# Kernel tuning notes

Measured on AMD Instinct MI355X. Metric: run time of the kernel, lower is better.

The kernel has to match this reference:

```python
import jax, jax.numpy as jnp
import numpy as np

N_NODES = 100000
N_EDGES = 1600000
F_IN, F_HID, F_OUT = 128, 128, 16
NEG_SLOPE = 0.2


def _glorot(key, shape):
    fan = sum(shape)
    return jax.random.uniform(key, shape, jnp.float32, -1.0, 1.0) * jnp.sqrt(6.0 / fan)


def setup_inputs() -> dict:
    key = jax.random.key(0)
    ks = jax.random.split(key, 16)
    x = jax.random.normal(ks[0], (N_NODES, F_IN), jnp.float32)
    edge_index = jax.random.randint(ks[1], (2, N_EDGES), 0, N_NODES, jnp.int64)
    d1, d2, d3 = F_HID, F_HID // 2, F_OUT
    return {
        'x': x,
        'edge_index': edge_index,
        'W1': _glorot(ks[2], (F_IN, d1)), 'a_src1': _glorot(ks[3], (d1,)), 'a_dst1': _glorot(ks[4], (d1,)), 'b1': jnp.zeros((d1,), jnp.float32),
        'W2': _glorot(ks[5], (d1, d2)), 'a_src2': _glorot(ks[6], (d2,)), 'a_dst2': _glorot(ks[7], (d2,)), 'b2': jnp.zeros((d2,), jnp.float32),
        'W3': _glorot(ks[8], (d2, d3)), 'a_src3': _glorot(ks[9], (d3,)), 'a_dst3': _glorot(ks[10], (d3,)), 'b3': jnp.zeros((d3,), jnp.float32),
    }


def gat_conv(x, src, dst, W, a_s, a_d, b):
    # x: [N, Fin] -> h: [N, Fout]; src/dst: [E] (self-loops included)
    h = x @ W
    e = jax.nn.leaky_relu(h @ a_s, NEG_SLOPE * 0 + NEG_SLOPE)  # placeholder avoided below
    # attention logits per edge: leaky_relu(alpha_src[src] + alpha_dst[dst])
    al_s = h @ a_s  # [N]
    al_d = h @ a_d  # [N]
    logits = jax.nn.leaky_relu(al_s[src] + al_d[dst], NEG_SLOPE)  # [E]
    # numerically stable softmax over incoming edges of each dst node
    m = jax.ops.segment_max(logits, dst, num_segments=N_NODES)
    m = jnp.where(jnp.isfinite(m), m, 0.0)
    ex = jnp.exp(logits - m[dst])
    denom = jax.ops.segment_sum(ex, dst, num_segments=N_NODES)
    alpha = ex / denom[dst]  # self-loops guarantee denom > 0
    out = jax.ops.segment_sum(alpha[:, None] * h[src], dst, num_segments=N_NODES)
    return out + b


def reference(x, edge_index, W1, a_src1, a_dst1, b1, W2, a_src2, a_dst2, b2, W3, a_src3, a_dst3, b3):
    loops = jnp.arange(N_NODES, dtype=edge_index.dtype)
    src = jnp.concatenate([edge_index[0], loops])
    dst = jnp.concatenate([edge_index[1], loops])
    h = gat_conv(x, src, dst, W1, a_src1, a_dst1, b1)
    h = jax.nn.relu(h)  # dropout p=0.5 is identity in eval mode
    h = gat_conv(h, src, dst, W2, a_src2, a_dst2, b2)
    h = jax.nn.relu(h)
    out = gat_conv(h, src, dst, W3, a_src3, a_dst3, b3)
    return out
```

## Files before the change

kernel.cpp:

```cpp
#include <hip/hip_runtime.h>
#include <hip/hip_bf16.h>

typedef __hip_bfloat16 bf16;
typedef __attribute__((ext_vector_type(8))) __bf16 bf16x8;
typedef __attribute__((ext_vector_type(4))) float f32x4;

static constexpr int N = 100000;
static constexpr int E = 1600000;
static constexpr int ETOT = E + N;
static constexpr float SLOPE = 0.2f;

__device__ __constant__ int c_poff[12] = {0, 16384, 16512, 16640,
                                          16768, 24960, 25024, 25088,
                                          25152, 26176, 26192, 26208};
static constexpr int PTOT = 26224;
static constexpr int H_POFF[12] = {0, 16384, 16512, 16640, 16768, 24960,
                                   25024, 25088, 25152, 26176, 26192, 26208};

struct Src12 { const void* p[12]; };

__device__ __forceinline__ float bfLo(unsigned u) { return __uint_as_float(u << 16); }
__device__ __forceinline__ float bfHi(unsigned u) { return __uint_as_float(u & 0xFFFF0000u); }

__device__ __forceinline__ void fma8(const uint4 r, float e, float* acc) {
  acc[0] = fmaf(e, bfLo(r.x), acc[0]);
  acc[1] = fmaf(e, bfHi(r.x), acc[1]);
  acc[2] = fmaf(e, bfLo(r.y), acc[2]);
  acc[3] = fmaf(e, bfHi(r.y), acc[3]);
  acc[4] = fmaf(e, bfLo(r.z), acc[4]);
  acc[5] = fmaf(e, bfHi(r.z), acc[5]);
  acc[6] = fmaf(e, bfLo(r.w), acc[6]);
  acc[7] = fmaf(e, bfHi(r.w), acc[7]);
}

__device__ __forceinline__ float edge_ex(float l) {
  l = (l > 0.f) ? l : SLOPE * l;
  return __expf(l);
}

__device__ __forceinline__ void loadEdge(const int* __restrict__ ei32,
                                         const long long* __restrict__ ei64,
                                         int use64, int t, int& s, int& d) {
  if (t >= E) { s = d = t - E; return; }
  if (use64) { s = (int)ei64[t]; d = (int)ei64[E + t]; }
  else       { s = ei32[t];      d = ei32[E + t]; }
}

__device__ __forceinline__ unsigned pk2(float a, float b) {
  bf16 x = __float2bfloat16(a), y = __float2bfloat16(b);
  unsigned short ux = *(unsigned short*)&x, uy = *(unsigned short*)&y;
  return ((unsigned)uy << 16) | ux;
}

static constexpr int CHUNK = 8192;
static constexpr int NCHK  = (ETOT + CHUNK - 1) / CHUNK;
static constexpr int NB1   = (N + 511) / 512;
static constexpr int M1    = NB1 * NCHK;
static constexpr int SBLK  = (M1 + 255) / 256;

__global__ __launch_bounds__(256) void detect_kernel(
    const unsigned long long* __restrict__ ei64,
    const unsigned short* __restrict__ w1u16, int* __restrict__ flags) {
  const int t = threadIdx.x;
  __shared__ unsigned long long bl[4];
  __shared__ unsigned long long sb64;
  const int w = t >> 6;
  bool p64 = (t < 64) && (ei64[t] >= (unsigned long long)N);
  unsigned long long b64 = __ballot(p64);
  if (t == 0) sb64 = b64;
  bool pf = (((w1u16[t] >> 7) & 0xFFu) >= 126u);
  unsigned long long bf_ = __ballot(pf);
  if ((t & 63) == 0) bl[w] = bf_;
  __syncthreads();
  if (t == 0) {
    flags[0] = (sb64 == 0ull) ? 1 : 0;
    flags[1] = ((bl[0] | bl[1] | bl[2] | bl[3]) != 0ull) ? 1 : 0;
  }
}

static constexpr int PB_PAR = (PTOT + 255) / 256;
static constexpr int PB_W1  = 128 * 128 / 256;
static constexpr int PB_W2  = 128 * 64 / 256;
static constexpr int PB_W3  = 64 * 16 / 256;
static constexpr int PB_TOT = NCHK + PB_PAR + PB_W1 + PB_W2 + PB_W3;

__device__ __forceinline__ void conv_w(const void* W, int kd, int dout, int f32,
                                       bf16* __restrict__ wt, int idx) {
  int n = idx / kd, k = idx - n * kd;
  float v = f32 ? ((const float*)W)[k * dout + n]
                : __bfloat162float(((const bf16*)W)[k * dout + n]);
  wt[idx] = __float2bfloat16(v);
}

__global__ __launch_bounds__(256) void prep_kernel(
    const int* __restrict__ ei32, const long long* __restrict__ ei64,
    const int* __restrict__ flags, int* __restrict__ c1,
    Src12 s, float* __restrict__ prm,
    bf16* __restrict__ w1t, bf16* __restrict__ w2t, bf16* __restrict__ w3t) {
  const int b = blockIdx.x, tid = threadIdx.x;
  const int f64 = flags[0], f32 = flags[1];
  if (b < NCHK) {
    __shared__ int h1[NB1];
    if (tid < NB1) h1[tid] = 0;
    __syncthreads();
    const int t0 = b * CHUNK;
#pragma unroll 4
    for (int i = tid; i < CHUNK; i += 256) {
      int t = t0 + i;
      if (t < ETOT) {
        int d = (t >= E) ? (t - E) : (f64 ? (int)ei64[E + t] : ei32[E + t]);
        atomicAdd(&h1[d >> 9], 1);
      }
    }
    __syncthreads();
    if (tid < NB1) c1[tid * NCHK + b] = h1[tid];
  } else if (b < NCHK + PB_PAR) {
    int t = (b - NCHK) * 256 + tid;
    if (t < PTOT) {
      int k = 0;
#pragma unroll
      for (int i = 1; i < 12; ++i)
        if (t >= c_poff[i]) k = i;
      int j = t - c_poff[k];
      prm[t] = f32 ? ((const float*)s.p[k])[j]
                   : __bfloat162float(((const bf16*)s.p[k])[j]);
    }
  } else if (b < NCHK + PB_PAR + PB_W1) {
    conv_w(s.p[0], 128, 128, f32, w1t, (b - NCHK - PB_PAR) * 256 + tid);
  } else if (b < NCHK + PB_PAR + PB_W1 + PB_W2) {
    conv_w(s.p[4], 128, 64, f32, w2t, (b - NCHK - PB_PAR - PB_W1) * 256 + tid);
  } else {
    conv_w(s.p[8], 64, 16, f32, w3t, (b - NCHK - PB_PAR - PB_W1 - PB_W2) * 256 + tid);
  }
}

__global__ __launch_bounds__(256) void scanA_kernel(const int* __restrict__ c1,
                                                    int* __restrict__ bsum) {
  __shared__ int red[256];
  const int t = threadIdx.x;
  const int i = blockIdx.x * 256 + t;
  red[t] = (i < M1) ? c1[i] : 0;
  __syncthreads();
#pragma unroll
  for (int off = 128; off > 0; off >>= 1) {
    if (t < off) red[t] += red[t + off];
    __syncthreads();
  }
  if (t == 0) bsum[blockIdx.x] = red[0];
}

__global__ __launch_bounds__(256) void scanB_kernel(const int* __restrict__ bsum,
                                                    int* __restrict__ boff) {
  __shared__ int s[256];
  const int t = threadIdx.x;
  const int v = (t < SBLK) ? bsum[t] : 0;
  s[t] = v;
  __syncthreads();
  for (int off = 1; off < 256; off <<= 1) {
    int u = (t >= off) ? s[t - off] : 0;
    __syncthreads();
    s[t] += u;
    __syncthreads();
  }
  if (t < SBLK) boff[t] = s[t] - v;
}

__global__ __launch_bounds__(256) void scanC_kernel(const int* __restrict__ c1,
                                                    const int* __restrict__ boff,
                                                    int* __restrict__ off1) {
  __shared__ int s[256];
  const int t = threadIdx.x;
  const int i = blockIdx.x * 256 + t;
  const int v = (i < M1) ? c1[i] : 0;
  s[t] = v;
  __syncthreads();
#pragma unroll
  for (int off = 1; off < 256; off <<= 1) {
    int u = (t >= off) ? s[t - off] : 0;
    __syncthreads();
    s[t] += u;
    __syncthreads();
  }
  if (i < M1) off1[i] = boff[blockIdx.x] + s[t] - v;
}

__device__ __forceinline__ void phaseC_body(int c, const int* __restrict__ ei32,
                                            const long long* __restrict__ ei64,
                                            int f64, const int* __restrict__ off1,
                                            int2* __restrict__ tmp) {
  __shared__ int cur[NB1];
  const int tid = threadIdx.x;
  if (tid < NB1) cur[tid] = off1[tid * NCHK + c];
  __syncthreads();
  const int t0 = c * CHUNK;
#pragma unroll 4
  for (int i = tid; i < CHUNK; i += 256) {
    int t = t0 + i;
    if (t < ETOT) {
      int s, d;
      loadEdge(ei32, ei64, f64, t, s, d);
      int pos = atomicAdd(&cur[d >> 9], 1);
      tmp[pos] = make_int2(d, s);
    }
  }
}

__global__ __launch_bounds__(256) void phaseD_kernel(const int* __restrict__ off1,
                                                     const int2* __restrict__ tmp,
                                                     int* __restrict__ rowptr,
                                                     int* __restrict__ ssrt,
                                                     const float* __restrict__ als1,
                                                     const float* __restrict__ ald1,
                                                     float* __restrict__ exf) {
  __shared__ int h2[512], e2[512], cur[512];
  __shared__ int ps[256];
  const int b = blockIdx.x, t = threadIdx.x;
  const int base = off1[b * NCHK];
  const int end = (b + 1 < NB1) ? off1[(b + 1) * NCHK] : ETOT;
  const int len = end - base;
  h2[2 * t] = 0; h2[2 * t + 1] = 0;
  __syncthreads();
  for (int i = t; i < len; i += 256)
    atomicAdd(&h2[tmp[base + i].x & 511], 1);
  __syncthreads();
  const int s1 = h2[2 * t], s2 = h2[2 * t + 1];
  ps[t] = s1 + s2;
  __syncthreads();
  for (int off = 1; off < 256; off <<= 1) {
    int u = (t >= off) ? ps[t - off] : 0;
    __syncthreads();
    ps[t] += u;
    __syncthreads();
  }
  const int ep = ps[t] - (s1 + s2);
  e2[2 * t] = ep;
  e2[2 * t + 1] = ep + s1;
  cur[2 * t] = ep;
  cur[2 * t + 1] = ep + s1;
  __syncthreads();
#pragma unroll
  for (int k = 0; k < 2; ++k) {
    int f = 2 * t + k;
    int node = (b << 9) + f;
    if (node < N) rowptr[node] = base + e2[f];
  }
  if (b == 0 && t == 0) rowptr[N] = ETOT;
  for (int i = t; i < len; i += 256) {
    int2 e = tmp[base + i];
    int pos = base + atomicAdd(&cur[e.x & 511], 1);
    ssrt[pos] = e.y;
    exf[pos] = edge_ex(als1[e.y] + ald1[e.x]);
  }
}

template <int KD, int DOUT, bool XD>
__device__ __forceinline__ void gemm_body(int bb, const void* __restrict__ inv,
                                          const int* __restrict__ flags,
                                          const unsigned short* __restrict__ wt,
                                          bf16* __restrict__ h,
                                          const float* __restrict__ a_s,
                                          const float* __restrict__ a_d,
                                          float* __restrict__ als,
                                          float* __restrict__ ald) {
  constexpr int SA = KD + 8;
  constexpr int NT = DOUT / 16;
  constexpr int KS = KD / 32;
  __shared__ unsigned short sA[64 * SA];
  __shared__ unsigned short sB[DOUT * SA];
  const int tid = threadIdx.x;
  const int m0 = bb * 64;
  for (int idx = tid; idx < DOUT * KD / 8; idx += 256) {
    int n = idx / (KD / 8), k8 = idx - n * (KD / 8);
    *(uint4*)(sB + n * SA + k8 * 8) = *(const uint4*)(wt + n * KD + k8 * 8);
  }
  const bool f32 = XD ? (flags[1] != 0) : false;
  for (int idx = tid; idx < 64 * KD / 8; idx += 256) {
    int r = idx / (KD / 8), k8 = idx - r * (KD / 8);
    int m = m0 + r;
    uint4 v = make_uint4(0, 0, 0, 0);
    if (m < N) {
      if (XD && f32) {
        const float4 v0 = *((const float4*)inv + ((size_t)m * KD + k8 * 8) / 4);
        const float4 v1 = *((const float4*)inv + ((size_t)m * KD + k8 * 8) / 4 + 1);
        v = make_uint4(pk2(v0.x, v0.y), pk2(v0.z, v0.w),
                       pk2(v1.x, v1.y), pk2(v1.z, v1.w));
      } else {
        v = *((const uint4*)inv + ((size_t)m * KD + k8 * 8) / 8);
      }
    }
    *(uint4*)(sA + r * SA + k8 * 8) = v;
  }
  __syncthreads();
  const int lane = tid & 63;
  const int wv = tid >> 6;
  const int lr = lane & 15;
  const int q = lane >> 4;
  f32x4 acc[NT];
#pragma unroll
  for (int t = 0; t < NT; ++t)
#pragma unroll
    for (int r = 0; r < 4; ++r) acc[t][r] = 0.f;
  const int arow = wv * 16 + lr;
#pragma unroll
  for (int ks = 0; ks < KS; ++ks) {
    const int k0 = ks * 32 + q * 8;
    const bf16x8 a = *(const bf16x8*)(sA + arow * SA + k0);
#pragma unroll
    for (int t = 0; t < NT; ++t) {
      const bf16x8 b = *(const bf16x8*)(sB + (t * 16 + lr) * SA + k0);
      acc[t] = __builtin_amdgcn_mfma_f32_16x16x32_bf16(a, b, acc[t], 0, 0, 0);
    }
  }
  float ps[4] = {0.f, 0.f, 0.f, 0.f}, pd[4] = {0.f, 0.f, 0.f, 0.f};
#pragma unroll
  for (int t = 0; t < NT; ++t) {
    const float av = a_s[t * 16 + lr];
    const float dv = a_d[t * 16 + lr];
#pragma unroll
    for (int r = 0; r < 4; ++r) {
      ps[r] = fmaf(acc[t][r], av, ps[r]);
      pd[r] = fmaf(acc[t][r], dv, pd[r]);
    }
  }
#pragma unroll
  for (int m = 1; m < 16; m <<= 1)
#pragma unroll
    for (int r = 0; r < 4; ++r) {
      ps[r] += __shfl_xor(ps[r], m, 64);
      pd[r] += __shfl_xor(pd[r], m, 64);
    }
  const int mb = m0 + wv * 16 + q * 4;
  if (lr == 0) {
#pragma unroll
    for (int r = 0; r < 4; ++r) {
      int m = mb + r;
      if (m < N) { als[m] = ps[r]; ald[m] = pd[r]; }
    }
  }
#pragma unroll
  for (int t = 0; t < NT; ++t)
#pragma unroll
    for (int r = 0; r < 4; ++r) {
      int m = mb + r;
      if (m < N) h[(size_t)m * DOUT + t * 16 + lr] = __float2bfloat16(acc[t][r]);
    }
}

static constexpr int GB1 = (N + 63) / 64;

__global__ __launch_bounds__(256) void gemm1_phaseC(
    const void* __restrict__ x, const int* __restrict__ flags,
    const unsigned short* __restrict__ wt, bf16* __restrict__ h,
    const float* __restrict__ a_s, const float* __restrict__ a_d,
    float* __restrict__ als, float* __restrict__ ald,
    const int* __restrict__ ei32, const long long* __restrict__ ei64,
    const int* __restrict__ off1, int2* __restrict__ tmp) {
  if (blockIdx.x < GB1) {
    gemm_body<128, 128, true>(blockIdx.x, x, flags, wt, h, a_s, a_d, als, ald);
  } else {
    int c = blockIdx.x - GB1;
    if (c < NCHK) phaseC_body(c, ei32, ei64, flags[0], off1, tmp);
  }
}

static constexpr int AB = (N + 127) / 128;

template <int DA, int DOUT, bool EXF>
__global__ __launch_bounds__(512) void aggemm_kernel(
    const int* __restrict__ rowptr, const int* __restrict__ ssrt,
    const float* __restrict__ exf,
    const float* __restrict__ als_in, const float* __restrict__ ald_in,
    const unsigned short* __restrict__ hin, const float* __restrict__ bias,
    const unsigned short* __restrict__ wt, bf16* __restrict__ hout,
    const float* __restrict__ a_s, const float* __restrict__ a_d,
    float* __restrict__ als_out, float* __restrict__ ald_out) {
  constexpr int SA = DA + 8;
  constexpr int TPN = DA / 8;
  constexpr int NPR = 512 / TPN;
  constexpr int NR = 128 / NPR;
  constexpr int NT = DOUT / 16;
  constexpr int KS = DA / 32;
  __shared__ unsigned short sA[128 * SA];
  const int tid = threadIdx.x;
  const int m0 = blockIdx.x * 128;
  const int sub = tid % TPN;
  const int rr0 = tid / TPN;
  const int col0 = sub * 8;
#pragma unroll
  for (int r = 0; r < NR; ++r) {
    const int row = r * NPR + rr0;
    const int d = m0 + row;
    if (d < N) {
      const int p0 = rowptr[d], p1 = rowptr[d + 1];
      const float ad = EXF ? 0.f : ald_in[d];
      float acc[8];
#pragma unroll
      for (int c = 0; c < 8; ++c) acc[c] = 0.f;
      float sum = 0.f;
      int p = p0;
      for (; p + 4 <= p1; p += 4) {
        const int s0 = ssrt[p + 0];
        const int s1 = ssrt[p + 1];
        const int s2 = ssrt[p + 2];
        const int s3 = ssrt[p + 3];
        const uint4 r0 = *reinterpret_cast<const uint4*>(hin + (size_t)s0 * DA + col0);
        const uint4 r1 = *reinterpret_cast<const uint4*>(hin + (size_t)s1 * DA + col0);
        const uint4 r2 = *reinterpret_cast<const uint4*>(hin + (size_t)s2 * DA + col0);
        const uint4 r3 = *reinterpret_cast<const uint4*>(hin + (size_t)s3 * DA + col0);
        const float x0 = EXF ? exf[p + 0] : edge_ex(als_in[s0] + ad);
        const float x1 = EXF ? exf[p + 1] : edge_ex(als_in[s1] + ad);
        const float x2 = EXF ? exf[p + 2] : edge_ex(als_in[s2] + ad);
        const float x3 = EXF ? exf[p + 3] : edge_ex(als_in[s3] + ad);
        sum += (x0 + x1) + (x2 + x3);
        fma8(r0, x0, acc);
        fma8(r1, x1, acc);
        fma8(r2, x2, acc);
        fma8(r3, x3, acc);
      }
      for (; p < p1; ++p) {
        const int s = ssrt[p];
        const uint4 rr = *reinterpret_cast<const uint4*>(hin + (size_t)s * DA + col0);
        const float x = EXF ? exf[p] : edge_ex(als_in[s] + ad);
        sum += x;
        fma8(rr, x, acc);
      }
      const float inv = 1.f / sum;
      float v[8];
#pragma unroll
      for (int c = 0; c < 8; ++c) {
        float w = acc[c] * inv + bias[col0 + c];
        v[c] = (w > 0.f) ? w : 0.f;
      }
      uint4 pk = make_uint4(pk2(v[0], v[1]), pk2(v[2], v[3]),
                            pk2(v[4], v[5]), pk2(v[6], v[7]));
      *(uint4*)(sA + row * SA + col0) = pk;
    }
  }
  __syncthreads();
  const int lane = tid & 63;
  const int wv = tid >> 6;
  const int lr = lane & 15;
  const int q = lane >> 4;
  f32x4 acc[NT];
#pragma unroll
  for (int t = 0; t < NT; ++t)
#pragma unroll
    for (int r = 0; r < 4; ++r) acc[t][r] = 0.f;
  const int arow = wv * 16 + lr;
#pragma unroll
  for (int ks = 0; ks < KS; ++ks) {
    const int k0 = ks * 32 + q * 8;
    const bf16x8 a = *(const bf16x8*)(sA + arow * SA + k0);
#pragma unroll
    for (int t = 0; t < NT; ++t) {
      const bf16x8 b = *(const bf16x8*)(wt + (t * 16 + lr) * DA + k0);
      acc[t] = __builtin_amdgcn_mfma_f32_16x16x32_bf16(a, b, acc[t], 0, 0, 0);
    }
  }
  float ps[4] = {0.f, 0.f, 0.f, 0.f}, pd[4] = {0.f, 0.f, 0.f, 0.f};
#pragma unroll
  for (int t = 0; t < NT; ++t) {
    const float av = a_s[t * 16 + lr];
    const float dv = a_d[t * 16 + lr];
#pragma unroll
    for (int r = 0; r < 4; ++r) {
      ps[r] = fmaf(acc[t][r], av, ps[r]);
      pd[r] = fmaf(acc[t][r], dv, pd[r]);
    }
  }
#pragma unroll
  for (int m = 1; m < 16; m <<= 1)
#pragma unroll
    for (int r = 0; r < 4; ++r) {
      ps[r] += __shfl_xor(ps[r], m, 64);
      pd[r] += __shfl_xor(pd[r], m, 64);
    }
  const int mb = m0 + wv * 16 + q * 4;
  if (lr == 0) {
#pragma unroll
    for (int r = 0; r < 4; ++r) {
      int m = mb + r;
      if (m < N) { als_out[m] = ps[r]; ald_out[m] = pd[r]; }
    }
  }
#pragma unroll
  for (int t = 0; t < NT; ++t)
#pragma unroll
    for (int r = 0; r < 4; ++r) {
      int m = mb + r;
      if (m < N) hout[(size_t)m * DOUT + t * 16 + lr] = __float2bfloat16(acc[t][r]);
    }
}

template <int DOUT>
__global__ __launch_bounds__(256) void agg_final(const int* __restrict__ rowptr,
                                                 const int* __restrict__ ssrt,
                                                 const float* __restrict__ als,
                                                 const float* __restrict__ ald,
                                                 const unsigned short* __restrict__ hb,
                                                 const float* __restrict__ bias,
                                                 void* __restrict__ outv,
                                                 const int* __restrict__ flags) {
  constexpr int TPN = DOUT / 8;
  constexpr int NPB = 256 / TPN;
  const int sub = threadIdx.x % TPN;
  const int d = blockIdx.x * NPB + threadIdx.x / TPN;
  if (d >= N) return;
  const int p0 = rowptr[d], p1 = rowptr[d + 1];
  const float ad = ald[d];
  const int col0 = sub * 8;
  float acc[8];
#pragma unroll
  for (int c = 0; c < 8; ++c) acc[c] = 0.f;
  float sum = 0.f;
  int p = p0;
  for (; p + 4 <= p1; p += 4) {
    const int s0 = ssrt[p + 0];
    const int s1 = ssrt[p + 1];
    const int s2 = ssrt[p + 2];
    const int s3 = ssrt[p + 3];
    const uint4 r0 = *reinterpret_cast<const uint4*>(hb + (size_t)s0 * DOUT + col0);
    const uint4 r1 = *reinterpret_cast<const uint4*>(hb + (size_t)s1 * DOUT + col0);
    const uint4 r2 = *reinterpret_cast<const uint4*>(hb + (size_t)s2 * DOUT + col0);
    const uint4 r3 = *reinterpret_cast<const uint4*>(hb + (size_t)s3 * DOUT + col0);
    const float x0 = edge_ex(als[s0] + ad);
    const float x1 = edge_ex(als[s1] + ad);
    const float x2 = edge_ex(als[s2] + ad);
    const float x3 = edge_ex(als[s3] + ad);
    sum += (x0 + x1) + (x2 + x3);
    fma8(r0, x0, acc);
    fma8(r1, x1, acc);
    fma8(r2, x2, acc);
    fma8(r3, x3, acc);
  }
  for (; p < p1; ++p) {
    const int s = ssrt[p];
    const uint4 r = *reinterpret_cast<const uint4*>(hb + (size_t)s * DOUT + col0);
    const float x = edge_ex(als[s] + ad);
    sum += x;
    fma8(r, x, acc);
  }
  const float inv = 1.f / sum;
  const bool f32o = flags[1] != 0;
#pragma unroll
  for (int c = 0; c < 8; ++c) {
    float v = acc[c] * inv + bias[col0 + c];
    if (f32o) ((float*)outv)[(size_t)d * DOUT + col0 + c] = v;
    else      ((bf16*)outv)[(size_t)d * DOUT + col0 + c] = __float2bfloat16(v);
  }
}

static inline size_t rup(size_t v) { return (v + 255) & ~(size_t)255; }

extern "C" void kernel_launch(void* const* d_in, const int* in_sizes, int n_in,
                              void* d_out, int out_size, void* d_ws, size_t ws_size,
                              hipStream_t stream) {
  const int* ei32 = (const int*)d_in[1];
  const long long* ei64 = (const long long*)d_in[1];

  char* p = (char*)d_ws;
  int*   flags  = (int*)p;   p += 256;
  float* prm    = (float*)p; p += rup((size_t)PTOT * 4);
  bf16*  w1t    = (bf16*)p;  p += rup((size_t)128 * 128 * 2);
  bf16*  w2t    = (bf16*)p;  p += rup((size_t)128 * 64 * 2);
  bf16*  w3t    = (bf16*)p;  p += rup((size_t)64 * 16 * 2);
  float* als1   = (float*)p; p += rup((size_t)N * 4);
  float* ald1   = (float*)p; p += rup((size_t)N * 4);
  float* als2   = (float*)p; p += rup((size_t)N * 4);
  float* ald2   = (float*)p; p += rup((size_t)N * 4);
  float* als3   = (float*)p; p += rup((size_t)N * 4);
  float* ald3   = (float*)p; p += rup((size_t)N * 4);
  int*   rowptr = (int*)p;   p += rup((size_t)(N + 1) * 4);
  int*   c1     = (int*)p;   p += rup((size_t)M1 * 4);
  int*   off1   = (int*)p;   p += rup((size_t)M1 * 4);
  int*   bsum   = (int*)p;   p += rup((size_t)SBLK * 4);
  int*   boff   = (int*)p;   p += rup((size_t)SBLK * 4);
  int2*  tmp    = (int2*)p;  p += rup((size_t)ETOT * 8);
  int*   ssrt   = (int*)p;   p += rup((size_t)ETOT * 4);
  float* exf    = (float*)p; p += rup((size_t)ETOT * 4);
  bf16*  h1     = (bf16*)p;  p += rup((size_t)N * 128 * 2);
  bf16*  h2     = (bf16*)p;  p += rup((size_t)N * 64 * 2);
  bf16*  h3     = (bf16*)p;

  Src12 s;
  for (int i = 0; i < 12; ++i) s.p[i] = d_in[2 + i];

  detect_kernel<<<1, 256, 0, stream>>>(
      (const unsigned long long*)d_in[1], (const unsigned short*)d_in[2], flags);
  prep_kernel<<<PB_TOT, 256, 0, stream>>>(ei32, ei64, flags, c1, s, prm, w1t, w2t, w3t);
  scanA_kernel<<<SBLK, 256, 0, stream>>>(c1, bsum);
  scanB_kernel<<<1, 256, 0, stream>>>(bsum, boff);
  scanC_kernel<<<SBLK, 256, 0, stream>>>(c1, boff, off1);

  const float *as1 = prm + H_POFF[1], *ad1 = prm + H_POFF[2], *b1 = prm + H_POFF[3];
  const float *as2 = prm + H_POFF[5], *ad2 = prm + H_POFF[6], *b2 = prm + H_POFF[7];
  const float *as3 = prm + H_POFF[9], *ad3 = prm + H_POFF[10], *b3 = prm + H_POFF[11];

  gemm1_phaseC<<<GB1 + NCHK, 256, 0, stream>>>(
      d_in[0], flags, (const unsigned short*)w1t, h1, as1, ad1, als1, ald1,
      ei32, ei64, off1, tmp);
  phaseD_kernel<<<NB1, 256, 0, stream>>>(off1, tmp, rowptr, ssrt, als1, ald1, exf);
  aggemm_kernel<128, 64, true><<<AB, 512, 0, stream>>>(
      rowptr, ssrt, exf, als1, ald1, (const unsigned short*)h1, b1,
      (const unsigned short*)w2t, h2, as2, ad2, als2, ald2);
  aggemm_kernel<64, 16, false><<<AB, 512, 0, stream>>>(
      rowptr, ssrt, nullptr, als2, ald2, (const unsigned short*)h2, b2,
      (const unsigned short*)w3t, h3, as3, ad3, als3, ald3);
  agg_final<16><<<(N + 127) / 128, 256, 0, stream>>>(
      rowptr, ssrt, als3, ald3, (const unsigned short*)h3, b3, d_out, flags);
}
```

Measured before the change: 345.2 us.

## Pack bucketed edges into 32-bit words and shrink aggregation blocks to 64 rows

The temporary bucketed edge array now stores the 9-bit local destination and a 17-bit source index in one 32-bit word instead of an int2, which halves the scatter writes and re-reads between phase C and phase D. Phase D also caches the bucket's destination attention values in shared memory, so it no longer gathers ald1 from global memory for every edge. The fused aggregate+GEMM kernels switch from 512-thread, 128-row blocks to 256-thread, 64-row blocks, giving more blocks and less shared memory per block. The packing assumes source indices fit in 17 bits, which holds because N is 100000.

```diff
diff --git a/kernel.cpp b/kernel.cpp
--- a/kernel.cpp
+++ b/kernel.cpp
@@ -187,7 +187,7 @@
 __device__ __forceinline__ void phaseC_body(int c, const int* __restrict__ ei32,
                                             const long long* __restrict__ ei64,
                                             int f64, const int* __restrict__ off1,
-                                            int2* __restrict__ tmp) {
+                                            unsigned* __restrict__ tmp) {
   __shared__ int cur[NB1];
   const int tid = threadIdx.x;
   if (tid < NB1) cur[tid] = off1[tid * NCHK + c];
@@ -200,28 +200,34 @@
       int s, d;
       loadEdge(ei32, ei64, f64, t, s, d);
       int pos = atomicAdd(&cur[d >> 9], 1);
-      tmp[pos] = make_int2(d, s);
+      tmp[pos] = ((unsigned)(d & 511) << 17) | (unsigned)s;
     }
   }
 }
 
 __global__ __launch_bounds__(256) void phaseD_kernel(const int* __restrict__ off1,
-                                                     const int2* __restrict__ tmp,
+                                                     const unsigned* __restrict__ tmp,
                                                      int* __restrict__ rowptr,
                                                      int* __restrict__ ssrt,
                                                      const float* __restrict__ als1,
                                                      const float* __restrict__ ald1,
                                                      float* __restrict__ exf) {
   __shared__ int h2[512], e2[512], cur[512];
+  __shared__ float alds[512];
   __shared__ int ps[256];
   const int b = blockIdx.x, t = threadIdx.x;
   const int base = off1[b * NCHK];
   const int end = (b + 1 < NB1) ? off1[(b + 1) * NCHK] : ETOT;
   const int len = end - base;
   h2[2 * t] = 0; h2[2 * t + 1] = 0;
+#pragma unroll
+  for (int k = 0; k < 2; ++k) {
+    int node = (b << 9) + 2 * t + k;
+    alds[2 * t + k] = (node < N) ? ald1[node] : 0.f;
+  }
   __syncthreads();
   for (int i = t; i < len; i += 256)
-    atomicAdd(&h2[tmp[base + i].x & 511], 1);
+    atomicAdd(&h2[tmp[base + i] >> 17], 1);
   __syncthreads();
   const int s1 = h2[2 * t], s2 = h2[2 * t + 1];
   ps[t] = s1 + s2;
@@ -246,10 +252,12 @@
   }
   if (b == 0 && t == 0) rowptr[N] = ETOT;
   for (int i = t; i < len; i += 256) {
-    int2 e = tmp[base + i];
-    int pos = base + atomicAdd(&cur[e.x & 511], 1);
-    ssrt[pos] = e.y;
-    exf[pos] = edge_ex(als1[e.y] + ald1[e.x]);
+    unsigned e = tmp[base + i];
+    int f = e >> 17;
+    int s = (int)(e & 0x1FFFFu);
+    int pos = base + atomicAdd(&cur[f], 1);
+    ssrt[pos] = s;
+    exf[pos] = edge_ex(als1[s] + alds[f]);
   }
 }
 
@@ -354,7 +362,7 @@
     const float* __restrict__ a_s, const float* __restrict__ a_d,
     float* __restrict__ als, float* __restrict__ ald,
     const int* __restrict__ ei32, const long long* __restrict__ ei64,
-    const int* __restrict__ off1, int2* __restrict__ tmp) {
+    const int* __restrict__ off1, unsigned* __restrict__ tmp) {
   if (blockIdx.x < GB1) {
     gemm_body<128, 128, true>(blockIdx.x, x, flags, wt, h, a_s, a_d, als, ald);
   } else {
@@ -363,10 +371,8 @@
   }
 }
 
-static constexpr int AB = (N + 127) / 128;
-
 template <int DA, int DOUT, bool EXF>
-__global__ __launch_bounds__(512) void aggemm_kernel(
+__global__ __launch_bounds__(256) void aggemm_kernel(
     const int* __restrict__ rowptr, const int* __restrict__ ssrt,
     const float* __restrict__ exf,
     const float* __restrict__ als_in, const float* __restrict__ ald_in,
@@ -376,13 +382,13 @@
     float* __restrict__ als_out, float* __restrict__ ald_out) {
   constexpr int SA = DA + 8;
   constexpr int TPN = DA / 8;
-  constexpr int NPR = 512 / TPN;
-  constexpr int NR = 128 / NPR;
+  constexpr int NPR = 256 / TPN;
+  constexpr int NR = 64 / NPR;
   constexpr int NT = DOUT / 16;
   constexpr int KS = DA / 32;
-  __shared__ unsigned short sA[128 * SA];
+  __shared__ unsigned short sA[64 * SA];
   const int tid = threadIdx.x;
-  const int m0 = blockIdx.x * 128;
+  const int m0 = blockIdx.x * 64;
   const int sub = tid % TPN;
   const int rr0 = tid / TPN;
   const int col0 = sub * 8;
@@ -559,28 +565,28 @@
   const long long* ei64 = (const long long*)d_in[1];
 
   char* p = (char*)d_ws;
-  int*   flags  = (int*)p;   p += 256;
-  float* prm    = (float*)p; p += rup((size_t)PTOT * 4);
-  bf16*  w1t    = (bf16*)p;  p += rup((size_t)128 * 128 * 2);
-  bf16*  w2t    = (bf16*)p;  p += rup((size_t)128 * 64 * 2);
-  bf16*  w3t    = (bf16*)p;  p += rup((size_t)64 * 16 * 2);
-  float* als1   = (float*)p; p += rup((size_t)N * 4);
-  float* ald1   = (float*)p; p += rup((size_t)N * 4);
-  float* als2   = (float*)p; p += rup((size_t)N * 4);
-  float* ald2   = (float*)p; p += rup((size_t)N * 4);
-  float* als3   = (float*)p; p += rup((size_t)N * 4);
-  float* ald3   = (float*)p; p += rup((size_t)N * 4);
-  int*   rowptr = (int*)p;   p += rup((size_t)(N + 1) * 4);
-  int*   c1     = (int*)p;   p += rup((size_t)M1 * 4);
-  int*   off1   = (int*)p;   p += rup((size_t)M1 * 4);
-  int*   bsum   = (int*)p;   p += rup((size_t)SBLK * 4);
-  int*   boff   = (int*)p;   p += rup((size_t)SBLK * 4);
-  int2*  tmp    = (int2*)p;  p += rup((size_t)ETOT * 8);
-  int*   ssrt   = (int*)p;   p += rup((size_t)ETOT * 4);
-  float* exf    = (float*)p; p += rup((size_t)ETOT * 4);
-  bf16*  h1     = (bf16*)p;  p += rup((size_t)N * 128 * 2);
-  bf16*  h2     = (bf16*)p;  p += rup((size_t)N * 64 * 2);
-  bf16*  h3     = (bf16*)p;
+  int*      flags  = (int*)p;      p += 256;
+  float*    prm    = (float*)p;    p += rup((size_t)PTOT * 4);
+  bf16*     w1t    = (bf16*)p;     p += rup((size_t)128 * 128 * 2);
+  bf16*     w2t    = (bf16*)p;     p += rup((size_t)128 * 64 * 2);
+  bf16*     w3t    = (bf16*)p;     p += rup((size_t)64 * 16 * 2);
+  float*    als1   = (float*)p;    p += rup((size_t)N * 4);
+  float*    ald1   = (float*)p;    p += rup((size_t)N * 4);
+  float*    als2   = (float*)p;    p += rup((size_t)N * 4);
+  float*    ald2   = (float*)p;    p += rup((size_t)N * 4);
+  float*    als3   = (float*)p;    p += rup((size_t)N * 4);
+  float*    ald3   = (float*)p;    p += rup((size_t)N * 4);
+  int*      rowptr = (int*)p;      p += rup((size_t)(N + 1) * 4);
+  int*      c1     = (int*)p;      p += rup((size_t)M1 * 4);
+  int*      off1   = (int*)p;      p += rup((size_t)M1 * 4);
+  int*      bsum   = (int*)p;      p += rup((size_t)SBLK * 4);
+  int*      boff   = (int*)p;      p += rup((size_t)SBLK * 4);
+  unsigned* tmp    = (unsigned*)p; p += rup((size_t)ETOT * 4);
+  int*      ssrt   = (int*)p;      p += rup((size_t)ETOT * 4);
+  float*    exf    = (float*)p;    p += rup((size_t)ETOT * 4);
+  bf16*     h1     = (bf16*)p;     p += rup((size_t)N * 128 * 2);
+  bf16*     h2     = (bf16*)p;     p += rup((size_t)N * 64 * 2);
+  bf16*     h3     = (bf16*)p;
 
   Src12 s;
   for (int i = 0; i < 12; ++i) s.p[i] = d_in[2 + i];
@@ -600,10 +606,10 @@
       d_in[0], flags, (const unsigned short*)w1t, h1, as1, ad1, als1, ald1,
       ei32, ei64, off1, tmp);
   phaseD_kernel<<<NB1, 256, 0, stream>>>(off1, tmp, rowptr, ssrt, als1, ald1, exf);
-  aggemm_kernel<128, 64, true><<<AB, 512, 0, stream>>>(
+  aggemm_kernel<128, 64, true><<<GB1, 256, 0, stream>>>(
       rowptr, ssrt, exf, als1, ald1, (const unsigned short*)h1, b1,
       (const unsigned short*)w2t, h2, as2, ad2, als2, ald2);
-  aggemm_kernel<64, 16, false><<<AB, 512, 0, stream>>>(
+  aggemm_kernel<64, 16, false><<<GB1, 256, 0, stream>>>(
       rowptr, ssrt, nullptr, als2, ald2, (const unsigned short*)h2, b2,
       (const unsigned short*)w3t, h3, as3, ad3, als3, ald3);
   agg_final<16><<<(N + 127) / 128, 256, 0, stream>>>(
```

After: 355.7 us. +3.0%, slower.
